# Optimization experiments

Measured on AMD Instinct MI355X. Metric: run time of the kernel, lower is better.

Reference implementation:

```python
import jax, jax.numpy as jnp
import numpy as np

N_NODES, N_HYPER, N_SEMA, D, L, E, NB = 100000, 20000, 10, 64, 2, 1000000, 50000
EPS = 1e-9


def setup_inputs() -> dict:
    key = jax.random.key(0)
    ks = jax.random.split(key, 20)
    s = 1.0 / np.sqrt(D)
    inp = {
        "node_emb": jax.random.normal(ks[0], (N_NODES, D), jnp.float32) * 0.1,
        "hyper_emb": jax.random.normal(ks[1], (N_HYPER, D), jnp.float32) * 0.1,
        "sema_emb": jax.random.normal(ks[2], (N_SEMA, D), jnp.float32) * 0.1,
        "W_msg": jax.random.normal(ks[3], (L, D, D), jnp.float32) * s,
        "W_att": jax.random.normal(ks[4], (L, D, D), jnp.float32) * s,
        "W_upd": jax.random.normal(ks[5], (L, D, D), jnp.float32) * s,
        "Wi1": jax.random.normal(ks[6], (L, D, D), jnp.float32) * s,
        "Wi2": jax.random.normal(ks[7], (L, D, D), jnp.float32) * s,
        "Wo_n": jax.random.normal(ks[8], (L, D, D), jnp.float32) * s,
        "Wo_e": jax.random.normal(ks[9], (L, D, D), jnp.float32) * s,
        "Wo_s": jax.random.normal(ks[10], (L, D, D), jnp.float32) * s,
        "node_indices": jax.random.randint(ks[11], (NB,), 0, N_NODES, jnp.int32),
        "hyperedge_indices": jax.random.randint(ks[12], (N_HYPER,), 0, N_HYPER, jnp.int32),
        "semalink_indices": jnp.arange(N_SEMA, dtype=jnp.int32),
        "semalinks": jnp.stack(
            [
                jax.random.randint(ks[13], (E,), 0, N_NODES, jnp.int32),
                jax.random.randint(ks[14], (E,), 0, N_HYPER, jnp.int32),
                jax.random.randint(ks[15], (E,), 0, N_SEMA, jnp.int32),
            ],
            axis=1,
        ),
    }
    return inp


def reference(node_emb, hyper_emb, sema_emb, W_msg, W_att, W_upd, Wi1, Wi2,
              Wo_n, Wo_e, Wo_s, node_indices, hyperedge_indices,
              semalink_indices, semalinks):
    N, d = node_emb.shape
    H = hyper_emb.shape[0]
    n_layers = W_msg.shape[0]

    # torch.isin(semalinks[:,0], node_indices) as a fixed-shape membership mask
    member = jnp.zeros((N,), bool).at[node_indices].set(True)
    src = semalinks[:, 0]   # node id per semalink
    hed = semalinks[:, 1]   # hyperedge id per semalink
    sem = semalinks[:, 2]   # semantic/relation id per semalink
    mask = member[src]      # [E] bool, replaces dynamic filtering
    maskf = mask.astype(node_emb.dtype)

    ne, he = node_emb, hyper_emb
    for i in range(n_layers):
        # --- SemalinkAttentiveAggregator: edge->hyperedge attentive scatter ---
        m = (ne[src] + sema_emb[sem]) @ W_msg[i]              # [E, d]
        q = he[hed] @ W_att[i]                                # [E, d]
        logits = jnp.where(mask, jnp.sum(m * q, axis=-1), -1e30)
        lmax = jax.ops.segment_max(logits, hed, num_segments=H)
        lmax = jnp.where(jnp.isfinite(lmax), lmax, 0.0)
        w = jnp.exp(logits - lmax[hed]) * maskf               # [E]
        denom = jax.ops.segment_sum(w, hed, num_segments=H)
        agg = jax.ops.segment_sum(w[:, None] * m, hed, num_segments=H)
        agg = agg / (denom[:, None] + EPS)
        new_he = jnp.tanh(agg @ W_upd[i])
        cnt_h = jax.ops.segment_sum(maskf, hed, num_segments=H)
        # scatter update: only hyperedges that received messages
        he = jnp.where((cnt_h > 0)[:, None], new_he, he)

        # --- InnerPropagation: node <- mean of incident hyperedges ---
        hmsg = he[hed] * maskf[:, None]                       # [E, d]
        n_sum = jax.ops.segment_sum(hmsg, src, num_segments=N)
        n_cnt = jax.ops.segment_sum(maskf, src, num_segments=N)
        n_agg = n_sum / (n_cnt[:, None] + EPS)                # [N, d]
        ne_inner = jax.nn.leaky_relu(ne @ Wi1[i] + n_agg @ Wi2[i])

        # --- OuterPropagation: relation-modulated hyperedge->node messages ---
        omsg = (he[hed] * sema_emb[sem]) * maskf[:, None]     # [E, d]
        o_agg = jax.ops.segment_sum(omsg, src, num_segments=N)
        o_agg = o_agg / (n_cnt[:, None] + EPS)
        ne = jnp.tanh(ne_inner @ Wo_n[i] + o_agg @ Wo_e[i] + n_agg @ Wo_s[i])

    # in-place scatter of updated minibatch node embeddings
    node_out = node_emb.at[node_indices].set(ne[node_indices])
    return node_out, he
```

## Files before the change

kernel.cpp:

```cpp
#include <hip/hip_runtime.h>
#include <cmath>


#define EPSF 1e-9f
#define NSLOT 40960
#define SENT 0xFFFFFFFFu
#define ATP 68
typedef unsigned long long ull;

__device__ __forceinline__ float group16_sum(float v){
  v += __shfl_xor(v, 1, 64);
  v += __shfl_xor(v, 2, 64);
  v += __shfl_xor(v, 4, 64);
  v += __shfl_xor(v, 8, 64);
  return v;
}
__device__ __forceinline__ float xgroup_sum(float v){
  v += __shfl_xor(v, 16, 64);
  v += __shfl_xor(v, 32, 64);
  return v;
}
__device__ __forceinline__ unsigned short f2bf(float f){
  unsigned b = __float_as_uint(f);
  unsigned r = (b + 0x7FFFu + ((b >> 16) & 1u)) >> 16;
  return (unsigned short)r;
}
__device__ __forceinline__ float bf2f(unsigned short u){
  return __uint_as_float(((unsigned)u) << 16);
}

__global__ __launch_bounds__(256) void k_copy4(const float4* __restrict__ in, float4* __restrict__ out, int n){
  int i = blockIdx.x*256 + threadIdx.x;
  if (i < n) out[i] = in[i];
}

__global__ __launch_bounds__(256) void k_set_member(const int* __restrict__ idx, int* __restrict__ member, int n){
  int i = blockIdx.x*256 + threadIdx.x;
  if (i < n) member[idx[i]] = 1;
}

__global__ __launch_bounds__(256) void k_build_list(int* __restrict__ member, int* __restrict__ mlist,
                                                    int* __restrict__ mcount, int N){
  int n = blockIdx.x*256 + threadIdx.x;
  if (n < N && member[n]) {
    int p = atomicAdd(mcount, 1);
    mlist[p] = n;
    member[n] = p + 2;
  }
}

__global__ __launch_bounds__(256) void k_count_rec(const int* __restrict__ sl, const int* __restrict__ member,
    ull* __restrict__ rec, int* __restrict__ cnt_hed, int* __restrict__ cnt_slot, int E){
  int e = blockIdx.x*256 + threadIdx.x;
  if (e >= E) return;
  int src = sl[3*e];
  int m = member[src];
  if (m){
    int slot = m - 2;
    int hed = sl[3*e+1];
    int sem = sl[3*e+2];
    unsigned lo = (unsigned)slot | ((unsigned)sem << 20);
    rec[e] = (ull)lo | ((ull)(unsigned)hed << 32);
    atomicAdd(&cnt_hed[hed], 1);
    atomicAdd(&cnt_slot[slot], 1);
  } else {
    rec[e] = (ull)SENT << 32;
  }
}

__global__ __launch_bounds__(256) void k_scan1(const int* __restrict__ in, int* __restrict__ out, int n,
                                               int* __restrict__ partials){
  __shared__ int s[256];
  int b = blockIdx.x, t = threadIdx.x;
  int base = b*2048 + t*8;
  int v[8]; int sum = 0;
  #pragma unroll
  for (int j=0;j<8;j++){ int i = base + j; v[j] = (i<n) ? in[i] : 0; sum += v[j]; }
  s[t] = sum;
  __syncthreads();
  for (int o=1;o<256;o<<=1){
    int x = (t>=o) ? s[t-o] : 0;
    __syncthreads();
    s[t] += x;
    __syncthreads();
  }
  int excl = s[t] - sum;
  if (t == 255) partials[b] = s[255];
  int run = excl;
  #pragma unroll
  for (int j=0;j<8;j++){ int i = base + j; if (i<n) out[i] = run; run += v[j]; }
}

__global__ void k_scan2(int* __restrict__ partials, int nb, int* __restrict__ out, int n){
  if (threadIdx.x==0 && blockIdx.x==0){
    int run = 0;
    for (int i=0;i<nb;i++){ int x = partials[i]; partials[i] = run; run += x; }
    out[n] = run;
  }
}

__global__ __launch_bounds__(256) void k_scan3(int* __restrict__ out, const int* __restrict__ partials, int n){
  int i = blockIdx.x*256 + threadIdx.x;
  if (i < n) out[i] += partials[i >> 11];
}

__global__ __launch_bounds__(256) void k_scatter_both(const ull* __restrict__ rec,
    const int* __restrict__ mcountp,
    const int* __restrict__ off_hed, int* __restrict__ cur_hed, unsigned* __restrict__ edge_hed,
    const int* __restrict__ off_slot, int* __restrict__ cur_slot, unsigned* __restrict__ edge_src, int E){
  int w = blockIdx.x & 7;
  int chunk = blockIdx.x >> 3;
  int nchunk = gridDim.x >> 3;
  int per = (E + nchunk - 1) / nchunk;
  int lo_i = chunk * per;
  int hi_i = min(E, lo_i + per);
  int divs = (*mcountp + 7) >> 3;
  for (int i = lo_i + threadIdx.x; i < hi_i; i += 256){
    ull r = rec[i];
    unsigned hed = (unsigned)(r >> 32);
    if (hed == SENT) continue;
    unsigned lo = (unsigned)r;
    int slot = lo & 0xFFFFF;
    if ((int)hed / 2500 == w){
      int p = off_hed[hed] + atomicAdd(&cur_hed[hed], 1);
      edge_hed[p] = lo;
    }
    if (slot / divs == w){
      int p = off_slot[slot] + atomicAdd(&cur_slot[slot], 1);
      edge_src[p] = hed | (lo & 0xFFF00000u);
    }
  }
}

#define LOAD_W(Wl, Wsrc) for (int i_=threadIdx.x; i_<1024; i_+=256) ((float4*)Wl)[i_] = ((const float4*)(Wsrc))[i_];

#define STAGE_AT(At, ro, nrows, LOADEXPR)                              \
  {                                                                    \
    int cg_ = threadIdx.x & 15, rl_ = threadIdx.x >> 4;                \
    for (int p_ = 0; p_ < 4; ++p_){                                    \
      int rloc_ = p_*16 + rl_;                                         \
      int r_ = (ro) + rloc_;                                           \
      float4 v_ = make_float4(0.f,0.f,0.f,0.f);                        \
      if (r_ < (nrows)){ v_ = (LOADEXPR); }                            \
      At[cg_*4+0][rloc_] = v_.x;                                       \
      At[cg_*4+1][rloc_] = v_.y;                                       \
      At[cg_*4+2][rloc_] = v_.z;                                       \
      At[cg_*4+3][rloc_] = v_.w;                                       \
    }                                                                  \
  }

__device__ __forceinline__ void gemm44(const float* __restrict__ Wl, const float (*At)[ATP],
                                       int rg4, int cg4, float4 acc[4]){
  #pragma unroll 8
  for (int k = 0; k < 64; ++k){
    const float4 w = *(const float4*)&Wl[k*64 + cg4];
    const float4 a = *(const float4*)&At[k][rg4];
    acc[0].x = fmaf(a.x,w.x,acc[0].x); acc[0].y = fmaf(a.x,w.y,acc[0].y);
    acc[0].z = fmaf(a.x,w.z,acc[0].z); acc[0].w = fmaf(a.x,w.w,acc[0].w);
    acc[1].x = fmaf(a.y,w.x,acc[1].x); acc[1].y = fmaf(a.y,w.y,acc[1].y);
    acc[1].z = fmaf(a.y,w.z,acc[1].z); acc[1].w = fmaf(a.y,w.w,acc[1].w);
    acc[2].x = fmaf(a.z,w.x,acc[2].x); acc[2].y = fmaf(a.z,w.y,acc[2].y);
    acc[2].z = fmaf(a.z,w.z,acc[2].z); acc[2].w = fmaf(a.z,w.w,acc[2].w);
    acc[3].x = fmaf(a.w,w.x,acc[3].x); acc[3].y = fmaf(a.w,w.y,acc[3].y);
    acc[3].z = fmaf(a.w,w.z,acc[3].z); acc[3].w = fmaf(a.w,w.w,acc[3].w);
  }
}

#define ZERO4(a) { a[0]=make_float4(0,0,0,0); a[1]=make_float4(0,0,0,0); a[2]=make_float4(0,0,0,0); a[3]=make_float4(0,0,0,0); }

__global__ __launch_bounds__(256) void k_rowmatA(const float* __restrict__ ne, const float* __restrict__ Wm,
    const float* __restrict__ Wi1, const int* __restrict__ mlist, const int* __restrict__ mcountp,
    unsigned short* __restrict__ nm_bf, float* __restrict__ inner1){
  __shared__ float W1[4096], W2[4096];
  __shared__ float At[64][ATP];
  int t = threadIdx.x;
  int nrows = *mcountp;
  int ntiles = (nrows + 63) >> 6;
  LOAD_W(W1, Wm)
  LOAD_W(W2, Wi1)
  int cg4 = (t & 15)*4, rg4 = (t >> 4)*4;
  for (int tile = blockIdx.x; tile < ntiles; tile += gridDim.x){
    int ro = tile << 6;
    __syncthreads();
    STAGE_AT(At, ro, nrows, (*(const float4*)&ne[(size_t)mlist[r_]*64 + cg_*4]))
    __syncthreads();
    float4 a1[4]; ZERO4(a1)
    float4 a2[4]; ZERO4(a2)
    #pragma unroll 4
    for (int k = 0; k < 64; ++k){
      const float4 w1 = *(const float4*)&W1[k*64 + cg4];
      const float4 w2 = *(const float4*)&W2[k*64 + cg4];
      const float4 a  = *(const float4*)&At[k][rg4];
      a1[0].x=fmaf(a.x,w1.x,a1[0].x); a1[0].y=fmaf(a.x,w1.y,a1[0].y); a1[0].z=fmaf(a.x,w1.z,a1[0].z); a1[0].w=fmaf(a.x,w1.w,a1[0].w);
      a1[1].x=fmaf(a.y,w1.x,a1[1].x); a1[1].y=fmaf(a.y,w1.y,a1[1].y); a1[1].z=fmaf(a.y,w1.z,a1[1].z); a1[1].w=fmaf(a.y,w1.w,a1[1].w);
      a1[2].x=fmaf(a.z,w1.x,a1[2].x); a1[2].y=fmaf(a.z,w1.y,a1[2].y); a1[2].z=fmaf(a.z,w1.z,a1[2].z); a1[2].w=fmaf(a.z,w1.w,a1[2].w);
      a1[3].x=fmaf(a.w,w1.x,a1[3].x); a1[3].y=fmaf(a.w,w1.y,a1[3].y); a1[3].z=fmaf(a.w,w1.z,a1[3].z); a1[3].w=fmaf(a.w,w1.w,a1[3].w);
      a2[0].x=fmaf(a.x,w2.x,a2[0].x); a2[0].y=fmaf(a.x,w2.y,a2[0].y); a2[0].z=fmaf(a.x,w2.z,a2[0].z); a2[0].w=fmaf(a.x,w2.w,a2[0].w);
      a2[1].x=fmaf(a.y,w2.x,a2[1].x); a2[1].y=fmaf(a.y,w2.y,a2[1].y); a2[1].z=fmaf(a.y,w2.z,a2[1].z); a2[1].w=fmaf(a.y,w2.w,a2[1].w);
      a2[2].x=fmaf(a.z,w2.x,a2[2].x); a2[2].y=fmaf(a.z,w2.y,a2[2].y); a2[2].z=fmaf(a.z,w2.z,a2[2].z); a2[2].w=fmaf(a.z,w2.w,a2[2].w);
      a2[3].x=fmaf(a.w,w2.x,a2[3].x); a2[3].y=fmaf(a.w,w2.y,a2[3].y); a2[3].z=fmaf(a.w,w2.z,a2[3].z); a2[3].w=fmaf(a.w,w2.w,a2[3].w);
    }
    #pragma unroll
    for (int i = 0; i < 4; ++i){
      int r = ro + rg4 + i;
      if (r < nrows){
        ushort4 s;
        s.x = f2bf(a1[i].x); s.y = f2bf(a1[i].y); s.z = f2bf(a1[i].z); s.w = f2bf(a1[i].w);
        *(ushort4*)&nm_bf[(size_t)r*64 + cg4] = s;
        *(float4*)&inner1[(size_t)r*64 + cg4] = a2[i];
      }
    }
  }
}

__global__ __launch_bounds__(256) void k_rowmatB(const float* __restrict__ he, const float* __restrict__ sema,
    const float* __restrict__ Wa, const float* __restrict__ Wm,
    float* __restrict__ hq, float* __restrict__ smbuf, int H, int NS_){
  __shared__ float W1[4096];
  __shared__ float At[64][ATP];
  int t = threadIdx.x;
  if (blockIdx.x == 0 && t < 160){
    int sr = t >> 4, c4 = (t & 15)*4;
    float4 accs = make_float4(0,0,0,0);
    #pragma unroll 8
    for (int k = 0; k < 64; ++k){
      float a = sema[sr*64 + k];
      float4 w = *(const float4*)&Wm[k*64 + c4];
      accs.x = fmaf(a,w.x,accs.x); accs.y = fmaf(a,w.y,accs.y);
      accs.z = fmaf(a,w.z,accs.z); accs.w = fmaf(a,w.w,accs.w);
    }
    *(float4*)&smbuf[(size_t)sr*64 + c4] = accs;
  }
  LOAD_W(W1, Wa)
  int nrows = H;
  int ntiles = (nrows + 63) >> 6;
  int cg4 = (t & 15)*4, rg4 = (t >> 4)*4;
  for (int tile = blockIdx.x; tile < ntiles; tile += gridDim.x){
    int ro = tile << 6;
    __syncthreads();
    STAGE_AT(At, ro, nrows, (*(const float4*)&he[(size_t)r_*64 + cg_*4]))
    __syncthreads();
    float4 acc[4]; ZERO4(acc)
    gemm44(W1, At, rg4, cg4, acc);
    #pragma unroll
    for (int i = 0; i < 4; ++i){
      int r = ro + rg4 + i;
      if (r < nrows) *(float4*)&hq[(size_t)r*64 + cg4] = acc[i];
    }
  }
}

__global__ __launch_bounds__(256) void k_matfuse(const float* __restrict__ inner1, const float* __restrict__ nagg,
    const float* __restrict__ oagg, const float* __restrict__ Wi2, const float* __restrict__ Wn,
    const float* __restrict__ We, const float* __restrict__ Ws,
    const int* __restrict__ mlist, const int* __restrict__ mcountp, float* __restrict__ ne){
  __shared__ float Wl[4096];
  __shared__ float At[64][ATP];
  int t = threadIdx.x;
  int cnt = *mcountp;
  int ntiles = (cnt + 63) >> 6;
  int cg4 = (t & 15)*4, rg4 = (t >> 4)*4;
  for (int tile = blockIdx.x; tile < ntiles; tile += gridDim.x){
    int ro = tile << 6;
    __syncthreads();
    STAGE_AT(At, ro, cnt, (*(const float4*)&nagg[(size_t)r_*64 + cg_*4]))
    LOAD_W(Wl, Ws)
    __syncthreads();
    float4 acc[4]; ZERO4(acc)
    gemm44(Wl, At, rg4, cg4, acc);
    __syncthreads();
    LOAD_W(Wl, Wi2)
    __syncthreads();
    float4 p1[4]; ZERO4(p1)
    gemm44(Wl, At, rg4, cg4, p1);
    float x[4][4];
    #pragma unroll
    for (int i = 0; i < 4; ++i){
      int r = ro + rg4 + i;
      float4 v = make_float4(0.f,0.f,0.f,0.f);
      if (r < cnt) v = *(const float4*)&inner1[(size_t)r*64 + cg4];
      float x0 = p1[i].x + v.x, x1 = p1[i].y + v.y, x2 = p1[i].z + v.z, x3 = p1[i].w + v.w;
      x[i][0] = x0 >= 0.f ? x0 : 0.01f*x0;
      x[i][1] = x1 >= 0.f ? x1 : 0.01f*x1;
      x[i][2] = x2 >= 0.f ? x2 : 0.01f*x2;
      x[i][3] = x3 >= 0.f ? x3 : 0.01f*x3;
    }
    __syncthreads();
    #pragma unroll
    for (int i = 0; i < 4; ++i)
      #pragma unroll
      for (int j = 0; j < 4; ++j)
        At[cg4+j][rg4+i] = x[i][j];
    LOAD_W(Wl, Wn)
    __syncthreads();
    gemm44(Wl, At, rg4, cg4, acc);
    __syncthreads();
    STAGE_AT(At, ro, cnt, (*(const float4*)&oagg[(size_t)r_*64 + cg_*4]))
    LOAD_W(Wl, We)
    __syncthreads();
    gemm44(Wl, At, rg4, cg4, acc);
    #pragma unroll
    for (int i = 0; i < 4; ++i){
      int r = ro + rg4 + i;
      if (r < cnt){
        float4 o = make_float4(tanhf(acc[i].x), tanhf(acc[i].y), tanhf(acc[i].z), tanhf(acc[i].w));
        *(float4*)&ne[(size_t)mlist[r]*64 + cg4] = o;
      }
    }
  }
}

__global__ __launch_bounds__(256) void k_attn_upd(const int* __restrict__ off_hed, const unsigned* __restrict__ edge_hed,
    const unsigned short* __restrict__ nm_bf, const float* __restrict__ smb, const float* __restrict__ hq,
    const float* __restrict__ W, const float* __restrict__ he_cur, float* __restrict__ he_next,
    unsigned short* __restrict__ he_bf, int H){
  __shared__ float Wl[4096];
  __shared__ float sm_lds[640];
  __shared__ float aggl[256];
  int t = threadIdx.x;
  for (int i=t;i<1024;i+=256) ((float4*)Wl)[i] = ((const float4*)W)[i];
  for (int i=t;i<640;i+=256) sm_lds[i] = smb[i];
  __syncthreads();
  int w = t >> 6, lane = t & 63;
  int nhb = (H + 3) >> 2;
  for (int hb = blockIdx.x; hb < nhb; hb += gridDim.x){
    int h = hb*4 + w;
    if (h >= H) continue;
    int start = off_hed[h], end = off_hed[h+1];
    if (start == end){
      float v = he_cur[(size_t)h*64 + lane];
      he_next[(size_t)h*64 + lane] = v;
      he_bf[(size_t)h*64 + lane] = f2bf(v);
      continue;
    }
    int g = lane >> 4, dl = (lane & 15)*4;
    float4 q4 = *(const float4*)&hq[(size_t)h*64 + dl];
    float ax=0.f, ay=0.f, az=0.f, aw=0.f, dsum=0.f, m=-3.4e38f;
    for (int idx0 = start; idx0 < end; idx0 += 4){
      int idx = idx0 + g;
      bool valid = idx < end;
      unsigned u = valid ? edge_hed[idx] : 0u;
      int slot = u & 0xFFFFF, sem = u >> 20;
      float4 nm4 = make_float4(0.f,0.f,0.f,0.f);
      if (valid){
        ushort4 nu = *(const ushort4*)&nm_bf[(size_t)slot*64 + dl];
        nm4 = make_float4(bf2f(nu.x), bf2f(nu.y), bf2f(nu.z), bf2f(nu.w));
      }
      float4 sm4 = *(const float4*)&sm_lds[sem*64 + dl];
      float mkx = nm4.x+sm4.x, mky = nm4.y+sm4.y, mkz = nm4.z+sm4.z, mkw = nm4.w+sm4.w;
      float part = mkx*q4.x + mky*q4.y + mkz*q4.z + mkw*q4.w;
      part = group16_sum(part);
      float l = valid ? part : -3.4e38f;
      float mn = fmaxf(m, l);
      float scale = __expf(m - mn);
      float wgt = valid ? __expf(l - mn) : 0.f;
      ax = ax*scale + wgt*mkx; ay = ay*scale + wgt*mky;
      az = az*scale + wgt*mkz; aw = aw*scale + wgt*mkw;
      dsum = dsum*scale + wgt;
      m = mn;
    }
    float mg = fmaxf(m, __shfl_xor(m, 16, 64));
    mg = fmaxf(mg, __shfl_xor(mg, 32, 64));
    float cs = __expf(m - mg);
    ax*=cs; ay*=cs; az*=cs; aw*=cs; dsum*=cs;
    ax = xgroup_sum(ax); ay = xgroup_sum(ay); az = xgroup_sum(az); aw = xgroup_sum(aw);
    dsum = xgroup_sum(dsum);
    if (lane < 16){
      float inv = 1.f/(dsum + EPSF);
      aggl[w*64 + dl+0] = ax*inv;
      aggl[w*64 + dl+1] = ay*inv;
      aggl[w*64 + dl+2] = az*inv;
      aggl[w*64 + dl+3] = aw*inv;
    }
    float o = 0.f;
    #pragma unroll 8
    for (int j=0;j<64;j++) o = fmaf(aggl[w*64 + j], Wl[j*64 + lane], o);
    float ov = tanhf(o);
    he_next[(size_t)h*64 + lane] = ov;
    he_bf[(size_t)h*64 + lane] = f2bf(ov);
  }
}

__global__ __launch_bounds__(256) void k_nodeagg2(const int* __restrict__ mcountp,
    const int* __restrict__ off_slot, const unsigned* __restrict__ edge_src,
    const unsigned short* __restrict__ he_bf, const float* __restrict__ sema,
    float* __restrict__ nagg, float* __restrict__ oagg){
  __shared__ float sm_lds[640];
  int t = threadIdx.x;
  for (int i=t;i<640;i+=256) sm_lds[i] = sema[i];
  __syncthreads();
  int w = t >> 6, lane = t & 63;
  int mc = *mcountp;
  int npb = (mc + 3) >> 2;
  int g = lane >> 4, dl = (lane & 15)*4;
  for (int pb = blockIdx.x; pb < npb; pb += gridDim.x){
    int p = pb*4 + w;
    if (p >= mc) continue;
    int start = off_slot[p], end = off_slot[p+1];
    float anx=0.f, any_=0.f, anz=0.f, anw=0.f;
    float aox=0.f, aoy=0.f, aoz=0.f, aow=0.f;
    for (int idx0 = start; idx0 < end; idx0 += 4){
      int idx = idx0 + g;
      if (idx < end){
        unsigned u = edge_src[idx];
        int hd = u & 0xFFFFF, sem = u >> 20;
        ushort4 hu = *(const ushort4*)&he_bf[(size_t)hd*64 + dl];
        float4 hv = make_float4(bf2f(hu.x), bf2f(hu.y), bf2f(hu.z), bf2f(hu.w));
        float4 sv = *(const float4*)&sm_lds[sem*64 + dl];
        anx += hv.x; any_ += hv.y; anz += hv.z; anw += hv.w;
        aox = fmaf(hv.x, sv.x, aox); aoy = fmaf(hv.y, sv.y, aoy);
        aoz = fmaf(hv.z, sv.z, aoz); aow = fmaf(hv.w, sv.w, aow);
      }
    }
    anx = xgroup_sum(anx); any_ = xgroup_sum(any_); anz = xgroup_sum(anz); anw = xgroup_sum(anw);
    aox = xgroup_sum(aox); aoy = xgroup_sum(aoy); aoz = xgroup_sum(aoz); aow = xgroup_sum(aow);
    if (lane < 16){
      float inv = 1.f/((float)(end - start) + EPSF);
      *(float4*)&nagg[(size_t)p*64 + dl] = make_float4(anx*inv, any_*inv, anz*inv, anw*inv);
      *(float4*)&oagg[(size_t)p*64 + dl] = make_float4(aox*inv, aoy*inv, aoz*inv, aow*inv);
    }
  }
}

extern "C" void kernel_launch(void* const* d_in, const int* in_sizes, int n_in,
                              void* d_out, int out_size, void* d_ws, size_t ws_size,
                              hipStream_t stream)
{
  (void)in_sizes; (void)n_in; (void)out_size; (void)ws_size;
  const float* node_emb  = (const float*)d_in[0];
  const float* hyper_emb = (const float*)d_in[1];
  const float* sema_emb  = (const float*)d_in[2];
  const float* W_msg = (const float*)d_in[3];
  const float* W_att = (const float*)d_in[4];
  const float* W_upd = (const float*)d_in[5];
  const float* Wi1   = (const float*)d_in[6];
  const float* Wi2   = (const float*)d_in[7];
  const float* Wo_n  = (const float*)d_in[8];
  const float* Wo_e  = (const float*)d_in[9];
  const float* Wo_s  = (const float*)d_in[10];
  const int* node_indices = (const int*)d_in[11];
  const int* semalinks    = (const int*)d_in[14];

  constexpr int N = 100000, H = 20000, NS = 10, L = 2, E = 1000000, NB = 50000;

  float* out_ne = (float*)d_out;
  float* out_he = (float*)d_out + (size_t)N*64;

  char* wsp = (char*)d_ws;
  auto alloc = [&](size_t bytes)->char*{ char* p = wsp; wsp += (bytes + 255) & ~(size_t)255; return p; };
  char* zstart = wsp;
  int* member   = (int*)alloc((size_t)N*4);
  int* cnt_hed  = (int*)alloc((size_t)H*4);
  int* cnt_slot = (int*)alloc((size_t)NSLOT*4);
  int* cur_hed  = (int*)alloc((size_t)H*4);
  int* cur_slot = (int*)alloc((size_t)NSLOT*4);
  int* mcount   = (int*)alloc(256);
  size_t zbytes = (size_t)(wsp - zstart);
  int* off_hed   = (int*)alloc((size_t)(H+1)*4);
  int* off_slot  = (int*)alloc((size_t)(NSLOT+1)*4);
  int* mlist     = (int*)alloc((size_t)NB*4);
  int* partials  = (int*)alloc(256);
  ull* rec       = (ull*)alloc((size_t)E*8);
  unsigned* edge_hed = (unsigned*)alloc((size_t)E*4);
  unsigned* edge_src = (unsigned*)alloc((size_t)E*4);
  float* smbuf  = (float*)alloc((size_t)NS*64*4);
  float* hq     = (float*)alloc((size_t)H*64*4);
  unsigned short* nm_bf = (unsigned short*)alloc((size_t)NB*64*2);
  unsigned short* he_bf = (unsigned short*)alloc((size_t)H*64*2);
  float* he1    = (float*)alloc((size_t)H*64*4);
  float* naggb  = (float*)alloc((size_t)NB*64*4);
  float* oaggb  = (float*)alloc((size_t)NB*64*4);
  float* inner1 = (float*)alloc((size_t)NB*64*4);

  hipMemsetAsync(zstart, 0, zbytes, stream);

  k_copy4<<<(N*64/4 + 255)/256, 256, 0, stream>>>((const float4*)node_emb, (float4*)out_ne, N*64/4);
  k_set_member<<<(NB+255)/256, 256, 0, stream>>>(node_indices, member, NB);
  k_build_list<<<(N+255)/256, 256, 0, stream>>>(member, mlist, mcount, N);
  k_count_rec<<<(E+255)/256, 256, 0, stream>>>(semalinks, member, rec, cnt_hed, cnt_slot, E);

  int nb_h = (H + 2047)/2048, nb_s = (NSLOT + 2047)/2048;
  k_scan1<<<nb_h, 256, 0, stream>>>(cnt_hed, off_hed, H, partials);
  k_scan2<<<1, 64, 0, stream>>>(partials, nb_h, off_hed, H);
  k_scan3<<<(H+255)/256, 256, 0, stream>>>(off_hed, partials, H);
  k_scan1<<<nb_s, 256, 0, stream>>>(cnt_slot, off_slot, NSLOT, partials);
  k_scan2<<<1, 64, 0, stream>>>(partials, nb_s, off_slot, NSLOT);
  k_scan3<<<(NSLOT+255)/256, 256, 0, stream>>>(off_slot, partials, NSLOT);

  k_scatter_both<<<1024, 256, 0, stream>>>(rec, mcount, off_hed, cur_hed, edge_hed,
                                           off_slot, cur_slot, edge_src, E);

  for (int i = 0; i < L; ++i){
    const float* Wm = W_msg + (size_t)i*4096;
    const float* Wa = W_att + (size_t)i*4096;
    const float* Wu = W_upd + (size_t)i*4096;
    const float* wi1 = Wi1 + (size_t)i*4096;
    const float* wi2 = Wi2 + (size_t)i*4096;
    const float* won = Wo_n + (size_t)i*4096;
    const float* woe = Wo_e + (size_t)i*4096;
    const float* wos = Wo_s + (size_t)i*4096;
    const float* he_cur = (i == 0) ? hyper_emb : he1;
    float* he_next = (i == 0) ? he1 : out_he;

    k_rowmatA<<<800, 256, 0, stream>>>(out_ne, Wm, wi1, mlist, mcount, nm_bf, inner1);
    k_rowmatB<<<320, 256, 0, stream>>>(he_cur, sema_emb, Wa, Wm, hq, smbuf, H, NS);
    k_attn_upd<<<1280, 256, 0, stream>>>(off_hed, edge_hed, nm_bf, smbuf, hq, Wu, he_cur, he_next, he_bf, H);
    k_nodeagg2<<<1280, 256, 0, stream>>>(mcount, off_slot, edge_src, he_bf, sema_emb, naggb, oaggb);
    k_matfuse<<<800, 256, 0, stream>>>(inner1, naggb, oaggb, wi2, won, woe, wos, mlist, mcount, out_ne);
  }
}
```

Baseline: 363.0 us.

## Fuse hyperedge query projection into attention kernel and rebalance scatter partitioning

Removes the separate k_rowmatB launch. The attention kernel now computes sema@W_msg into shared memory per block and, for each non-empty hyperedge, computes its query vector he@W_att on the fly through a per-wave shared row. This drops the hq and smbuf global buffers and one launch per layer. The cost is that every one of the 1280 blocks recomputes the small sema projection, and the per-hyperedge query reads W_att from global or cache scalar-by-lane. Separately, the scatter kernel uses 4 partitions instead of 8 and launches twice as many blocks, which changes the atomic contention and redundant-read balance.

```diff
diff --git a/kernel.cpp b/kernel.cpp
--- a/kernel.cpp
+++ b/kernel.cpp
@@ -108,20 +108,20 @@
     const int* __restrict__ mcountp,
     const int* __restrict__ off_hed, int* __restrict__ cur_hed, unsigned* __restrict__ edge_hed,
     const int* __restrict__ off_slot, int* __restrict__ cur_slot, unsigned* __restrict__ edge_src, int E){
-  int w = blockIdx.x & 7;
-  int chunk = blockIdx.x >> 3;
-  int nchunk = gridDim.x >> 3;
+  int w = blockIdx.x & 3;
+  int chunk = blockIdx.x >> 2;
+  int nchunk = gridDim.x >> 2;
   int per = (E + nchunk - 1) / nchunk;
   int lo_i = chunk * per;
   int hi_i = min(E, lo_i + per);
-  int divs = (*mcountp + 7) >> 3;
+  int divs = (*mcountp + 3) >> 2;
   for (int i = lo_i + threadIdx.x; i < hi_i; i += 256){
     ull r = rec[i];
     unsigned hed = (unsigned)(r >> 32);
     if (hed == SENT) continue;
     unsigned lo = (unsigned)r;
     int slot = lo & 0xFFFFF;
-    if ((int)hed / 2500 == w){
+    if ((int)hed / 5000 == w){
       int p = off_hed[hed] + atomicAdd(&cur_hed[hed], 1);
       edge_hed[p] = lo;
     }
@@ -213,43 +213,6 @@
   }
 }
 
-__global__ __launch_bounds__(256) void k_rowmatB(const float* __restrict__ he, const float* __restrict__ sema,
-    const float* __restrict__ Wa, const float* __restrict__ Wm,
-    float* __restrict__ hq, float* __restrict__ smbuf, int H, int NS_){
-  __shared__ float W1[4096];
-  __shared__ float At[64][ATP];
-  int t = threadIdx.x;
-  if (blockIdx.x == 0 && t < 160){
-    int sr = t >> 4, c4 = (t & 15)*4;
-    float4 accs = make_float4(0,0,0,0);
-    #pragma unroll 8
-    for (int k = 0; k < 64; ++k){
-      float a = sema[sr*64 + k];
-      float4 w = *(const float4*)&Wm[k*64 + c4];
-      accs.x = fmaf(a,w.x,accs.x); accs.y = fmaf(a,w.y,accs.y);
-      accs.z = fmaf(a,w.z,accs.z); accs.w = fmaf(a,w.w,accs.w);
-    }
-    *(float4*)&smbuf[(size_t)sr*64 + c4] = accs;
-  }
-  LOAD_W(W1, Wa)
-  int nrows = H;
-  int ntiles = (nrows + 63) >> 6;
-  int cg4 = (t & 15)*4, rg4 = (t >> 4)*4;
-  for (int tile = blockIdx.x; tile < ntiles; tile += gridDim.x){
-    int ro = tile << 6;
-    __syncthreads();
-    STAGE_AT(At, ro, nrows, (*(const float4*)&he[(size_t)r_*64 + cg_*4]))
-    __syncthreads();
-    float4 acc[4]; ZERO4(acc)
-    gemm44(W1, At, rg4, cg4, acc);
-    #pragma unroll
-    for (int i = 0; i < 4; ++i){
-      int r = ro + rg4 + i;
-      if (r < nrows) *(float4*)&hq[(size_t)r*64 + cg4] = acc[i];
-    }
-  }
-}
-
 __global__ __launch_bounds__(256) void k_matfuse(const float* __restrict__ inner1, const float* __restrict__ nagg,
     const float* __restrict__ oagg, const float* __restrict__ Wi2, const float* __restrict__ Wn,
     const float* __restrict__ We, const float* __restrict__ Ws,
@@ -311,15 +274,29 @@
 }
 
 __global__ __launch_bounds__(256) void k_attn_upd(const int* __restrict__ off_hed, const unsigned* __restrict__ edge_hed,
-    const unsigned short* __restrict__ nm_bf, const float* __restrict__ smb, const float* __restrict__ hq,
-    const float* __restrict__ W, const float* __restrict__ he_cur, float* __restrict__ he_next,
+    const unsigned short* __restrict__ nm_bf, const float* __restrict__ sema, const float* __restrict__ Wm,
+    const float* __restrict__ Wa, const float* __restrict__ W,
+    const float* __restrict__ he_cur, float* __restrict__ he_next,
     unsigned short* __restrict__ he_bf, int H){
   __shared__ float Wl[4096];
   __shared__ float sm_lds[640];
   __shared__ float aggl[256];
+  __shared__ float hrow[4][64];
+  __shared__ float qh[4][64];
   int t = threadIdx.x;
   for (int i=t;i<1024;i+=256) ((float4*)Wl)[i] = ((const float4*)W)[i];
-  for (int i=t;i<640;i+=256) sm_lds[i] = smb[i];
+  if (t < 160){
+    int sr = t >> 4, c4 = (t & 15)*4;
+    float4 accs = make_float4(0,0,0,0);
+    #pragma unroll 8
+    for (int k = 0; k < 64; ++k){
+      float a = sema[sr*64 + k];
+      float4 wv = *(const float4*)&Wm[k*64 + c4];
+      accs.x = fmaf(a,wv.x,accs.x); accs.y = fmaf(a,wv.y,accs.y);
+      accs.z = fmaf(a,wv.z,accs.z); accs.w = fmaf(a,wv.w,accs.w);
+    }
+    *(float4*)&sm_lds[sr*64 + c4] = accs;
+  }
   __syncthreads();
   int w = t >> 6, lane = t & 63;
   int nhb = (H + 3) >> 2;
@@ -333,8 +310,13 @@
       he_bf[(size_t)h*64 + lane] = f2bf(v);
       continue;
     }
+    hrow[w][lane] = he_cur[(size_t)h*64 + lane];
+    float qv = 0.f;
+    #pragma unroll 8
+    for (int k = 0; k < 64; ++k) qv = fmaf(hrow[w][k], Wa[k*64 + lane], qv);
+    qh[w][lane] = qv;
     int g = lane >> 4, dl = (lane & 15)*4;
-    float4 q4 = *(const float4*)&hq[(size_t)h*64 + dl];
+    float4 q4 = *(const float4*)&qh[w][dl];
     float ax=0.f, ay=0.f, az=0.f, aw=0.f, dsum=0.f, m=-3.4e38f;
     for (int idx0 = start; idx0 < end; idx0 += 4){
       int idx = idx0 + g;
@@ -442,6 +424,7 @@
   const int* semalinks    = (const int*)d_in[14];
 
   constexpr int N = 100000, H = 20000, NS = 10, L = 2, E = 1000000, NB = 50000;
+  (void)NS;
 
   float* out_ne = (float*)d_out;
   float* out_he = (float*)d_out + (size_t)N*64;
@@ -463,8 +446,6 @@
   ull* rec       = (ull*)alloc((size_t)E*8);
   unsigned* edge_hed = (unsigned*)alloc((size_t)E*4);
   unsigned* edge_src = (unsigned*)alloc((size_t)E*4);
-  float* smbuf  = (float*)alloc((size_t)NS*64*4);
-  float* hq     = (float*)alloc((size_t)H*64*4);
   unsigned short* nm_bf = (unsigned short*)alloc((size_t)NB*64*2);
   unsigned short* he_bf = (unsigned short*)alloc((size_t)H*64*2);
   float* he1    = (float*)alloc((size_t)H*64*4);
@@ -487,7 +468,7 @@
   k_scan2<<<1, 64, 0, stream>>>(partials, nb_s, off_slot, NSLOT);
   k_scan3<<<(NSLOT+255)/256, 256, 0, stream>>>(off_slot, partials, NSLOT);
 
-  k_scatter_both<<<1024, 256, 0, stream>>>(rec, mcount, off_hed, cur_hed, edge_hed,
+  k_scatter_both<<<2048, 256, 0, stream>>>(rec, mcount, off_hed, cur_hed, edge_hed,
                                            off_slot, cur_slot, edge_src, E);
 
   for (int i = 0; i < L; ++i){
@@ -503,8 +484,8 @@
     float* he_next = (i == 0) ? he1 : out_he;
 
     k_rowmatA<<<800, 256, 0, stream>>>(out_ne, Wm, wi1, mlist, mcount, nm_bf, inner1);
-    k_rowmatB<<<320, 256, 0, stream>>>(he_cur, sema_emb, Wa, Wm, hq, smbuf, H, NS);
-    k_attn_upd<<<1280, 256, 0, stream>>>(off_hed, edge_hed, nm_bf, smbuf, hq, Wu, he_cur, he_next, he_bf, H);
+    k_attn_upd<<<1280, 256, 0, stream>>>(off_hed, edge_hed, nm_bf, sema_emb, Wm, Wa, Wu,
+                                         he_cur, he_next, he_bf, H);
     k_nodeagg2<<<1280, 256, 0, stream>>>(mcount, off_slot, edge_src, he_bf, sema_emb, naggb, oaggb);
     k_matfuse<<<800, 256, 0, stream>>>(inner1, naggb, oaggb, wi2, won, woe, wos, mlist, mcount, out_ne);
   }
```

Measured after the change: 374.0 us. +3.0%, slower.
